# Kernel optimization log

Hardware: AMD Instinct MI355X
Metric: run time of the kernel (lower is better)

## Reference

```python
import jax, jax.numpy as jnp
import numpy as np

B, N = 16, 2048
NOTE, BEAT_H, MEAS_H, FINAL_H = 512, 128, 64, 128
NUM_BEATS, NUM_MEAS = 256, 64
OUT = 11            # output_size; QPM_INDEX = 0
QPM = 0


def _uniform(k, shape, fan):
    b = 1.0 / np.sqrt(fan)
    return jax.random.uniform(k, shape, jnp.float32, -b, b)


def _lstm_cell(x, h, c, wih, whh, bih, bhh):
    g = x @ wih.T + bih + h @ whh.T + bhh
    ii, ff, gg, oo = jnp.split(g, 4, axis=-1)
    c2 = jax.nn.sigmoid(ff) * c + jax.nn.sigmoid(ii) * jnp.tanh(gg)
    return jax.nn.sigmoid(oo) * jnp.tanh(c2), c2


def setup_inputs() -> dict:
    key = jax.random.key(0)
    ks = jax.random.split(key, 20)
    note_emb = jax.random.normal(ks[0], (B, N, NOTE), jnp.float32)
    beat_emb = jax.random.normal(ks[1], (B, NUM_BEATS, BEAT_H), jnp.float32)
    measure_emb = jax.random.normal(ks[2], (B, NUM_MEAS, MEAS_H), jnp.float32)
    beat_numbers = jnp.sort(jax.random.randint(ks[3], (B, N), 0, NUM_BEATS), axis=1)
    measure_numbers = beat_numbers // (NUM_BEATS // NUM_MEAS)
    tin = BEAT_H + MEAS_H + 1 + (OUT - 1)   # beat-tempo LSTM input size
    fin = NOTE + BEAT_H + MEAS_H + OUT      # final LSTM input size
    d = OUT - 1
    return {
        "note_emb": note_emb, "beat_emb": beat_emb, "measure_emb": measure_emb,
        "beat_numbers": beat_numbers, "measure_numbers": measure_numbers,
        "Wa": _uniform(ks[4], (d, d), d), "ba": _uniform(ks[5], (d,), d),
        "ctx": _uniform(ks[6], (d,), d),
        "Wih_t": _uniform(ks[7], (4 * BEAT_H, tin), BEAT_H),
        "Whh_t": _uniform(ks[8], (4 * BEAT_H, BEAT_H), BEAT_H),
        "bih_t": _uniform(ks[9], (4 * BEAT_H,), BEAT_H),
        "bhh_t": _uniform(ks[10], (4 * BEAT_H,), BEAT_H),
        "Wih_f": _uniform(ks[11], (4 * FINAL_H, fin), FINAL_H),
        "Whh_f": _uniform(ks[12], (4 * FINAL_H, FINAL_H), FINAL_H),
        "bih_f": _uniform(ks[13], (4 * FINAL_H,), FINAL_H),
        "bhh_f": _uniform(ks[14], (4 * FINAL_H,), FINAL_H),
        "W_fc": _uniform(ks[15], (d, FINAL_H), FINAL_H),
        "b_fc": _uniform(ks[16], (d,), FINAL_H),
        "W_tfc": _uniform(ks[17], (1, BEAT_H), BEAT_H),
        "b_tfc": _uniform(ks[18], (1,), BEAT_H),
    }


def _decode(note_emb, beat_emb, measure_emb, beat_numbers, measure_numbers,
            Wa, ba, ctx, Wih_t, Whh_t, bih_t, bhh_t,
            Wih_f, Whh_f, bih_f, bhh_f, W_fc, b_fc, W_tfc, b_tfc):
    Bn, Nn = note_emb.shape[0], note_emb.shape[1]
    d = W_fc.shape[0]  # OUT - 1
    zs_beat = jnp.maximum(beat_numbers - beat_numbers[:, :1], 0)
    zs_meas = jnp.maximum(measure_numbers - measure_numbers[:, :1], 0)
    diff = jnp.diff(beat_numbers, axis=1)
    # beat_changed: first step forced to 1, then diff of beat numbers
    changed_all = jnp.concatenate([jnp.ones((Bn, 1), diff.dtype), diff], axis=1) > 0
    pos = jnp.arange(Nn)
    bidx = jnp.arange(Bn)

    carry0 = (
        jnp.zeros((Bn, BEAT_H)), jnp.zeros((Bn, BEAT_H)),        # tempo h, c
        jnp.zeros((Bn, FINAL_H)), jnp.zeros((Bn, FINAL_H)),      # final h, c
        jnp.zeros((Bn, d + 1)),                                   # prev_out
        jnp.zeros((Bn, beat_emb.shape[1], d)),                    # beat_results
        jnp.zeros((Bn, Nn, d + 1)),                               # out_total
    )

    def step(carry, i):
        th, tc, fh, fc_, prev_out, beat_results, out_total = carry
        changed = changed_all[:, i]                                # [B] bool
        # --- get_beat_corresp_out: notes j < i in the beat just finished ---
        prev_beat = beat_numbers[:, jnp.maximum(i - 1, 0)]         # [B]
        note_mask = (beat_numbers == prev_beat[:, None]) & (pos[None, :] < i)
        x = out_total[:, :, QPM + 1:]                              # [B,N,d]
        sim = (x @ Wa.T + ba) @ ctx                                # [B,N]
        sim = jnp.where(note_mask, sim, -1e9)
        w = jax.nn.softmax(sim, axis=1)
        result_node = jnp.einsum('bn,bnd->bd', w, x)
        result_node = jnp.where(note_mask.any(axis=1)[:, None], result_node, 0.0)
        cb = zs_beat[:, i]
        cm = zs_meas[:, i]
        # scatter result_node into beat_results only for batches whose beat changed
        old = beat_results[bidx, cb]
        beat_results = beat_results.at[bidx, cb].set(
            jnp.where(changed[:, None], result_node, old))
        # --- beat tempo RNN step (only applied where changed) ---
        tempo_in = jnp.concatenate([
            beat_emb[bidx, cb], measure_emb[bidx, cm],
            prev_out[:, QPM:QPM + 1], beat_results[bidx, cb]], axis=-1)
        th2, tc2 = _lstm_cell(tempo_in, th, tc, Wih_t, Whh_t, bih_t, bhh_t)
        th = jnp.where(changed[:, None], th2, th)
        tc = jnp.where(changed[:, None], tc2, tc)
        tmp_tempo = th2 @ W_tfc.T + b_tfc                          # [B,1]
        prev_out = prev_out.at[:, QPM:QPM + 1].set(
            jnp.where(changed[:, None], tmp_tempo, prev_out[:, QPM:QPM + 1]))
        # --- final note-level LSTM step (all batches) ---
        fin_in = jnp.concatenate([
            note_emb[:, i], beat_emb[bidx, cb], measure_emb[bidx, cm], prev_out], axis=-1)
        fh, fc_ = _lstm_cell(fin_in, fh, fc_, Wih_f, Whh_f, bih_f, bhh_f)
        out = fh @ W_fc.T + b_fc                                   # [B,d]
        prev_out = jnp.concatenate([prev_out[:, :QPM + 1], out], axis=-1)
        out_total = out_total.at[:, i].set(prev_out)
        return (th, tc, fh, fc_, prev_out, beat_results, out_total), None

    carry, _ = jax.lax.scan(step, carry0, jnp.arange(Nn))
    out_total = carry[-1]
    # zero out padded notes (note embedding all-zero rows)
    pad = (note_emb.sum(-1) == 0)[:, :, None]
    return jnp.where(pad, 0.0, out_total)


def reference(note_emb, beat_emb, measure_emb, beat_numbers, measure_numbers,
              Wa, ba, ctx, Wih_t, Whh_t, bih_t, bhh_t,
              Wih_f, Whh_f, bih_f, bhh_f, W_fc, b_fc, W_tfc, b_tfc):
    return _decode(note_emb, beat_emb, measure_emb, beat_numbers, measure_numbers,
                   Wa, ba, ctx, Wih_t, Whh_t, bih_t, bhh_t,
                   Wih_f, Whh_f, bih_f, bhh_f, W_fc, b_fc, W_tfc, b_tfc)
```

## Files before the change

### kernel.cpp

```cpp
#include <hip/hip_runtime.h>
#include <cstdint>
#include <cstddef>

#define B_      16
#define N_      2048
#define NOTE_   512
#define BEAT_H_ 128
#define MEAS_H_ 64
#define NBEATS_ 256
#define NMEAS_  64
#define OUT_    11
#define D_      10

typedef float f32x4 __attribute__((ext_vector_type(4)));
typedef unsigned int u32x4 __attribute__((ext_vector_type(4)));
typedef _Float16 h2v __attribute__((ext_vector_type(2)));

__device__ __forceinline__ float fexp2_(float x) {
#if __has_builtin(__builtin_amdgcn_exp2f)
    return __builtin_amdgcn_exp2f(x);
#else
    return exp2f(x);
#endif
}
__device__ __forceinline__ float frcp_(float x) {
#if __has_builtin(__builtin_amdgcn_rcpf)
    return __builtin_amdgcn_rcpf(x);
#else
    return 1.0f / x;
#endif
}
__device__ __forceinline__ float sigm_(float x) {
    return frcp_(1.0f + fexp2_(-1.4426950408889634f * x));
}
__device__ __forceinline__ float tanh_(float x) {
    return 1.0f - 2.0f * frcp_(fexp2_(2.8853900817779268f * x) + 1.0f);
}

__device__ __forceinline__ float dot2f_(unsigned wu, unsigned hu, float c) {
    union { unsigned u; h2v h; } a, bb;
    a.u = wu; bb.u = hu;
#if __has_builtin(__builtin_amdgcn_fdot2)
    return __builtin_amdgcn_fdot2(a.h, bb.h, c, false);
#else
    return c + (float)a.h[0] * (float)bb.h[0] + (float)a.h[1] * (float)bb.h[1];
#endif
}

#define BAR_LDS() asm volatile("s_waitcnt lgkmcnt(0)\n\ts_barrier" ::: "memory")

__device__ __forceinline__ void gstore16(void* p, _Float16 v) {
    *(__attribute__((address_space(1))) _Float16*)p = v;
}

__device__ __align__(16) _Float16 g_w_i16[512 * 128];
__device__ float g_bias_eff[512];
__device__ float g_wtail0[512];
__device__ __align__(16) _Float16 g_wht_i16[512 * 128];

__global__ __launch_bounds__(256) void pad_k(const float* __restrict__ note,
                                             int* __restrict__ padf) {
    int wave = threadIdx.x >> 6, lane = threadIdx.x & 63;
    int r = blockIdx.x * 4 + wave;
    const float* row = note + ((size_t)r << 9);
    float s = 0.f;
#pragma unroll
    for (int u = 0; u < 8; ++u) s += row[lane + (u << 6)];
#pragma unroll
    for (int off = 32; off; off >>= 1) s += __shfl_xor(s, off, 64);
    if (lane == 0) padf[r] = (s == 0.0f) ? 1 : 0;
}

__global__ __launch_bounds__(128) void fold_whh(
    const float* __restrict__ Whh_f, const float* __restrict__ Wih_f,
    const float* __restrict__ W_fc, const float* __restrict__ b_fc) {
    int gr = blockIdx.x;
    int t = threadIdx.x;
    __shared__ float tail[OUT_];
    if (t < OUT_) tail[t] = Wih_f[(size_t)gr * 715 + 704 + t];
    __syncthreads();
    float m = Whh_f[(size_t)gr * 128 + t];
#pragma unroll
    for (int d = 0; d < D_; ++d) m += tail[1 + d] * W_fc[d * 128 + t];
    int g = gr >> 7, e = gr & 127;
    int half = g >> 1, slot = g & 1;
    int gl = ((e >> 5) << 6) + (e & 31) + (half << 5);
    int k = slot * 16 + (t >> 3);
    g_w_i16[(size_t)(k * 256 + gl) * 8 + (t & 7)] = (_Float16)m;
    if (t == 0) {
        float bb = 0.f;
#pragma unroll
        for (int d = 0; d < D_; ++d) bb += tail[1 + d] * b_fc[d];
        g_bias_eff[gr] = bb;
        g_wtail0[gr] = tail[0];
    }
}

__global__ __launch_bounds__(128) void fold_wht(const float* __restrict__ Whh_t) {
    int gr = blockIdx.x, t = threadIdx.x;
    int g = gr >> 7, e = gr & 127;
    int half = g >> 1, slot = g & 1;
    int gl = ((e >> 5) << 6) + (e & 31) + (half << 5);
    int k = slot * 16 + (t >> 3);
    g_wht_i16[(size_t)(k * 256 + gl) * 8 + (t & 7)] = (_Float16)Whh_t[(size_t)gr * 128 + t];
}

__global__ __launch_bounds__(256) void tempo_pre_k(
    const float* __restrict__ beat, const float* __restrict__ meas,
    const int* __restrict__ bnum, const int* __restrict__ mnum,
    const float* __restrict__ Wih_t, const float* __restrict__ bih_t,
    const float* __restrict__ bhh_t, float* __restrict__ tpre) {
    __shared__ float sin_[16][192];
    int b = blockIdx.x, qt = blockIdx.y;
    int t = threadIdx.x;
    int bn0 = bnum[b << 11], mn0 = mnum[b << 11];
    for (int idx = t; idx < 16 * 192; idx += 256) {
        int qq = idx / 192, kk = idx - qq * 192;
        int q = qt * 16 + qq;
        float v;
        if (kk < 128) {
            v = beat[(size_t)(b * NBEATS_ + q) * 128 + kk];
        } else {
            int cm = ((q + bn0) >> 2) - mn0;
            if (cm > 63) cm = 63;
            if (cm < 0) cm = 0;
            v = meas[(size_t)(b * NMEAS_ + cm) * 64 + (kk - 128)];
        }
        sin_[qq][kk] = v;
    }
    __syncthreads();
    for (int half = 0; half < 2; ++half) {
        int c = t + half * 256;
        int j = ((c & 3) << 7) | (c >> 2);
        const float* wr = Wih_t + (size_t)j * 203;
        float bias = bih_t[j] + bhh_t[j];
        float acc[16] = {};
        for (int k = 0; k < 192; ++k) {
            float w = wr[k];
#pragma unroll
            for (int qq = 0; qq < 16; ++qq) acc[qq] += w * sin_[qq][k];
        }
        for (int qq = 0; qq < 16; ++qq)
            tpre[(size_t)(b * NBEATS_ + qt * 16 + qq) * 512 + c] = acc[qq] + bias;
    }
}

__global__ __launch_bounds__(256) void fin_pre_gemm(
    const float* __restrict__ note, const float* __restrict__ beat,
    const float* __restrict__ meas, const int* __restrict__ bnum,
    const int* __restrict__ mnum, const float* __restrict__ Wih_f,
    const float* __restrict__ bih_f, const float* __restrict__ bhh_f,
    float* __restrict__ finp) {
    __shared__ float As[16][64];
    __shared__ float Bs[16][64];
    int t = threadIdx.x;
    int r0 = blockIdx.x * 64;
    int j0 = blockIdx.y * 64;

    int am = t >> 2, alane = t & 3;
    int r = r0 + am;
    int b = r >> 11;
    int rb = b << 11;
    int cb = bnum[r] - bnum[rb];
    int cm = mnum[r] - mnum[rb];
    const float* arow_note = note + ((size_t)r << 9);
    const float* arow_beat = beat + ((size_t)(b * NBEATS_ + cb) << 7);
    const float* arow_meas = meas + ((size_t)(b * NMEAS_ + cm) << 6);

    int jj = t >> 2, blane = t & 3;
    int cB = j0 + jj;
    int jB = ((cB & 3) << 7) | (cB >> 2);
    const float* brow = Wih_f + (size_t)jB * 715;

    int tm0 = (t & 15) * 4, tn0 = (t >> 4) * 4;
    float acc[4][4] = {};

    for (int k0 = 0; k0 < 704; k0 += 16) {
        int ka = k0 + alane * 4;
        float4 av;
        if (ka < 512)      av = *(const float4*)(arow_note + ka);
        else if (ka < 640) av = *(const float4*)(arow_beat + (ka - 512));
        else               av = *(const float4*)(arow_meas + (ka - 640));
        int kb = k0 + blane * 4;
        float b0 = brow[kb], b1 = brow[kb + 1], b2 = brow[kb + 2], b3 = brow[kb + 3];
        __syncthreads();
        As[alane * 4 + 0][am] = av.x;
        As[alane * 4 + 1][am] = av.y;
        As[alane * 4 + 2][am] = av.z;
        As[alane * 4 + 3][am] = av.w;
        Bs[blane * 4 + 0][jj] = b0;
        Bs[blane * 4 + 1][jj] = b1;
        Bs[blane * 4 + 2][jj] = b2;
        Bs[blane * 4 + 3][jj] = b3;
        __syncthreads();
#pragma unroll
        for (int kk = 0; kk < 16; ++kk) {
            float4 a4 = *(const float4*)&As[kk][tm0];
            float4 b4 = *(const float4*)&Bs[kk][tn0];
            float aa[4] = {a4.x, a4.y, a4.z, a4.w};
            float bb[4] = {b4.x, b4.y, b4.z, b4.w};
#pragma unroll
            for (int mi = 0; mi < 4; ++mi)
#pragma unroll
                for (int ni = 0; ni < 4; ++ni) acc[mi][ni] += aa[mi] * bb[ni];
        }
    }
    float bias[4], beff[4];
#pragma unroll
    for (int ni = 0; ni < 4; ++ni) {
        int c = j0 + tn0 + ni;
        int j = ((c & 3) << 7) | (c >> 2);
        bias[ni] = bih_f[j] + bhh_f[j];
        beff[ni] = g_bias_eff[j];
    }
#pragma unroll
    for (int mi = 0; mi < 4; ++mi) {
        int rr = r0 + tm0 + mi;
        float eb = (rr & 2047) ? 1.0f : 0.0f;
        float4 o;
        o.x = acc[mi][0] + bias[0] + eb * beff[0];
        o.y = acc[mi][1] + bias[1] + eb * beff[1];
        o.z = acc[mi][2] + bias[2] + eb * beff[2];
        o.w = acc[mi][3] + bias[3] + eb * beff[3];
        *(float4*)(finp + ((size_t)rr << 9) + j0 + tn0) = o;
    }
}

__global__ __launch_bounds__(256)
__attribute__((amdgpu_waves_per_eu(1, 1)))
void decode_seq(
    float* finp,
    const float* __restrict__ tpre, const int* __restrict__ bnum,
    const float* __restrict__ Wih_t,
    const float* __restrict__ W_fc, const float* __restrict__ b_fc,
    const float* __restrict__ W_tfc, const float* __restrict__ b_tfc,
    const float* __restrict__ Wa, const float* __restrict__ ba,
    const float* __restrict__ ctx, float* __restrict__ tval) {
    __shared__ __align__(16) u32x4 wht_i_s[32 * 256];
    __shared__ __align__(16) _Float16 hbc16[2][128];
    __shared__ __align__(16) _Float16 ht16_s[128];
    __shared__ __align__(16) _Float16 u16_s[128];
    __shared__ __align__(16) float hA_s[128];
    __shared__ __align__(16) float s_w_s[1024];
    __shared__ float wfcT[128][12];
    __shared__ float bfc_s[12];
    __shared__ float v_s[12];
    __shared__ float cur_res[12];
    __shared__ float pred_s[4];
    __shared__ float sc_s[4];
    __shared__ unsigned short run_start_s[300];
    __shared__ short run_cb_s[300];
    __shared__ int nruns_s;

    const int t = threadIdx.x, l = t & 63, wid = t >> 6;
    const int b = blockIdx.x;
    const int half = l >> 5;
    const int e = wid * 32 + (l & 31);
    const int rowA = (half * 2) * 128 + e;
    const int rowB = (half * 2 + 1) * 128 + e;
    const float kmul = half ? 2.0f : 1.0f;
    const float badd = half ? -1.0f : 0.0f;

    const float* finb = finp + ((size_t)b << 11) * 512;
    char* hg = (char*)finb;
    const int colByte = (e << 4) + (half << 3);

    {
        const u32x4* src = (const u32x4*)g_wht_i16;
#pragma unroll
        for (int k2 = 0; k2 < 32; ++k2) wht_i_s[k2 * 256 + t] = src[k2 * 256 + t];
    }

    u32x4 wreg[32];
    {
        const u32x4* gw = (const u32x4*)g_w_i16;
#pragma unroll
        for (int k = 0; k < 32; ++k) wreg[k] = gw[k * 256 + t];
    }
    asm volatile("" : "+v"(wreg[0]), "+v"(wreg[1]), "+v"(wreg[2]), "+v"(wreg[3]),
                      "+v"(wreg[4]), "+v"(wreg[5]), "+v"(wreg[6]), "+v"(wreg[7]));
    asm volatile("" : "+v"(wreg[8]), "+v"(wreg[9]), "+v"(wreg[10]), "+v"(wreg[11]),
                      "+v"(wreg[12]), "+v"(wreg[13]), "+v"(wreg[14]), "+v"(wreg[15]));
    asm volatile("" : "+v"(wreg[16]), "+v"(wreg[17]), "+v"(wreg[18]), "+v"(wreg[19]),
                      "+v"(wreg[20]), "+v"(wreg[21]), "+v"(wreg[22]), "+v"(wreg[23]));
    asm volatile("" : "+v"(wreg[24]), "+v"(wreg[25]), "+v"(wreg[26]), "+v"(wreg[27]),
                      "+v"(wreg[28]), "+v"(wreg[29]), "+v"(wreg[30]), "+v"(wreg[31]));

    const float wt0A = g_wtail0[rowA];
    const float wt0B = g_wtail0[rowB];
    const float wtfc_r = W_tfc[e];
    const float btfc_r = b_tfc[0];
    float wiht0A = Wih_t[(size_t)rowA * 203 + 192];
    float wiht0B = Wih_t[(size_t)rowB * 203 + 192];
    float wihtdA[D_], wihtdB[D_];
#pragma unroll
    for (int d = 0; d < D_; ++d) {
        wihtdA[d] = Wih_t[(size_t)rowA * 203 + 193 + d];
        wihtdB[d] = Wih_t[(size_t)rowB * 203 + 193 + d];
    }

    for (int k = t; k < 128 * D_; k += 256) {
        int d = k >> 7, r = k & 127;
        wfcT[r][d] = W_fc[k];
    }
    if (t < 128) {
        hbc16[0][t] = (_Float16)0.f;
        hbc16[1][t] = (_Float16)0.f;
        ht16_s[t] = (_Float16)0.f;
    }
    if (t < D_) {
        bfc_s[t] = b_fc[t];
        cur_res[t] = 0.f;
        float vv = 0.f;
        for (int m = 0; m < D_; ++m) vv += ctx[m] * Wa[m * D_ + t];
        v_s[t] = vv;
    }
    if (t == 10) {
        float cc = 0.f;
        for (int m = 0; m < D_; ++m) cc += ba[m] * ctx[m];
        sc_s[0] = cc;
    }
    const int* bnb = bnum + (b << 11);
    int bn0 = bnb[0];
    int base = t * 8;
    int bv[8];
#pragma unroll
    for (int j = 0; j < 8; ++j) bv[j] = bnb[base + j];
    int prevv = base ? bnb[base - 1] : (bv[0] - 1);
    int c = 0;
    {
        int vv = prevv;
#pragma unroll
        for (int j = 0; j < 8; ++j) { c += (bv[j] != vv); vv = bv[j]; }
    }
    ((int*)s_w_s)[t] = c;
    __syncthreads();
    if (t == 0) {
        float c1v = sc_s[0];
        for (int d = 0; d < D_; ++d) c1v += bfc_s[d] * v_s[d];
        sc_s[3] = c1v;
    }
    if (t < 128) {
        float uu = 0.f;
#pragma unroll
        for (int d = 0; d < D_; ++d) uu += v_s[d] * wfcT[t][d];
        u16_s[t] = (_Float16)uu;
    }
    {
        int incl = c;
#pragma unroll
        for (int off = 1; off < 64; off <<= 1) {
            int n = __shfl_up(incl, off, 64);
            if (l >= off) incl += n;
        }
        if (l == 63) ((int*)s_w_s)[512 + wid] = incl;
        __syncthreads();
        int woff = 0;
        for (int w = 0; w < wid; ++w) woff += ((int*)s_w_s)[512 + w];
        int O = woff + incl - c;
        int vv = prevv;
#pragma unroll
        for (int j = 0; j < 8; ++j) {
            if (bv[j] != vv) {
                run_start_s[O] = (unsigned short)(base + j);
                run_cb_s[O] = (short)(bv[j] - bn0);
                O++;
            }
            vv = bv[j];
        }
        if (t == 0)
            nruns_s = ((int*)s_w_s)[512] + ((int*)s_w_s)[513] +
                      ((int*)s_w_s)[514] + ((int*)s_w_s)[515];
    }
    __syncthreads();
    const int nruns_r = nruns_s;

    float2 gf_cur = *(const float2*)((const char*)finb + colByte);
    float2 tp_cur = *(const float2*)((const char*)(tpre + (size_t)(b * NBEATS_) * 512) + colByte);
    int cur_run = -1, next_start = 0, run_s = 0, S_prev = 0;
    int pb = 0;
    float cf_r = 0.f, ct_r = 0.f;
    float prev0_r = 0.f;

#pragma unroll 1
    for (int i = 0; i < N_; ++i) {
        const bool changed = (i == next_start);
        if (changed) {
            ++cur_run;
            S_prev = run_s;
            run_s = i;
            next_start = (cur_run + 1 < nruns_r) ? (int)run_start_s[cur_run + 1] : (N_ * 2);
        }
        int inx = (i + 1 < N_) ? (i + 1) : i;
        float2 gf_nxt = *(const float2*)((const char*)finb + (size_t)inx * 2048 + colByte);

        float a0 = 0.f, a1 = 0.f, a2 = 0.f, a3 = 0.f;
        float b0 = 0.f, b1 = 0.f, b2 = 0.f, b3 = 0.f;
        {
            const u32x4* hq = (const u32x4*)&hbc16[pb][0];
#pragma unroll
            for (int k = 0; k < 16; ++k) {
                u32x4 H = hq[k];
                a0 = dot2f_(wreg[k].x, H.x, a0);
                a1 = dot2f_(wreg[k].y, H.y, a1);
                a2 = dot2f_(wreg[k].z, H.z, a2);
                a3 = dot2f_(wreg[k].w, H.w, a3);
                b0 = dot2f_(wreg[16 + k].x, H.x, b0);
                b1 = dot2f_(wreg[16 + k].y, H.y, b1);
                b2 = dot2f_(wreg[16 + k].z, H.z, b2);
                b3 = dot2f_(wreg[16 + k].w, H.w, b3);
            }
        }
        const float baseA = gf_cur.x + ((a0 + a1) + (a2 + a3));
        const float baseB = gf_cur.y + ((b0 + b1) + (b2 + b3));
        gf_cur = gf_nxt;
        float gA, gB, tv;

        if (!changed) {
            gA = baseA + wt0A * prev0_r;
            gB = baseB + wt0B * prev0_r;
            tv = prev0_r;
        } else {
            float t0 = 0.f, t1 = 0.f, t2 = 0.f, t3 = 0.f;
            float u0 = 0.f, u1 = 0.f, u2 = 0.f, u3 = 0.f;
            {
                const u32x4* htq = (const u32x4*)ht16_s;
#pragma unroll
                for (int k = 0; k < 16; ++k) {
                    u32x4 HT = htq[k];
                    u32x4 WA = wht_i_s[k * 256 + t];
                    u32x4 WB = wht_i_s[(16 + k) * 256 + t];
                    t0 = dot2f_(WA.x, HT.x, t0);
                    t1 = dot2f_(WA.y, HT.y, t1);
                    t2 = dot2f_(WA.z, HT.z, t2);
                    t3 = dot2f_(WA.w, HT.w, t3);
                    u0 = dot2f_(WB.x, HT.x, u0);
                    u1 = dot2f_(WB.y, HT.y, u1);
                    u2 = dot2f_(WB.z, HT.z, u2);
                    u3 = dot2f_(WB.w, HT.w, u3);
                }
            }
            float gtA = tp_cur.x + ((t0 + t1) + (t2 + t3)) + wiht0A * prev0_r;
            float gtB = tp_cur.y + ((u0 + u1) + (u2 + u3)) + wiht0B * prev0_r;
            if (cur_run + 1 < nruns_r) {
                int cb2 = (int)run_cb_s[cur_run + 1];
                tp_cur = *(const float2*)((const char*)(tpre + (size_t)(b * NBEATS_ + cb2) * 512) + colByte);
            }

            if (wid == 0) {
                int Lc = i - S_prev;
                if (Lc > 1024) Lc = 1024;
                const char* hgB = hg + (size_t)S_prev * 2048;
                const float c1 = sc_s[3];
                float lmax = -1e30f;
                for (int j = l; j < Lc; j += 64) {
                    const u32x4* hrow = (const u32x4*)(hgB + (size_t)j * 2048);
                    const u32x4* uq = (const u32x4*)u16_s;
                    float s0 = 0.f, s1 = 0.f, s2 = 0.f, s3 = 0.f;
#pragma unroll
                    for (int k = 0; k < 16; ++k) {
                        u32x4 hv = hrow[k], uv = uq[k];
                        s0 = dot2f_(hv.x, uv.x, s0);
                        s1 = dot2f_(hv.y, uv.y, s1);
                        s2 = dot2f_(hv.z, uv.z, s2);
                        s3 = dot2f_(hv.w, uv.w, s3);
                    }
                    float s = c1 + ((s0 + s1) + (s2 + s3));
                    s_w_s[j] = s;
                    lmax = fmaxf(lmax, s);
                }
#pragma unroll
                for (int off = 32; off; off >>= 1)
                    lmax = fmaxf(lmax, __shfl_xor(lmax, off, 64));
                float lsum = 0.f;
                for (int j = l; j < Lc; j += 64) {
                    float w = fexp2_(1.4426950408889634f * (s_w_s[j] - lmax));
                    s_w_s[j] = w;
                    lsum += w;
                }
#pragma unroll
                for (int off = 32; off; off >>= 1) lsum += __shfl_xor(lsum, off, 64);
                float inv = (Lc > 0) ? (1.0f / lsum) : 0.f;
                float hA0 = 0.f, hA1 = 0.f;
                for (int j = 0; j < Lc; ++j) {
                    unsigned hv = *(const unsigned*)(hgB + (size_t)j * 2048 + (l << 2));
                    float w = s_w_s[j];
                    union { unsigned u; _Float16 h[2]; } hu; hu.u = hv;
                    hA0 += w * (float)hu.h[0];
                    hA1 += w * (float)hu.h[1];
                }
                hA_s[2 * l] = hA0 * inv;
                hA_s[2 * l + 1] = hA1 * inv;
                int dd = l >> 3, rl = l & 7, d2 = 8 + dd;
                float po1 = 0.f, po2 = 0.f;
                for (int k2 = 0; k2 < 16; ++k2) {
                    int r = rl + (k2 << 3);
                    float hv = hA_s[r];
                    po1 += hv * wfcT[r][dd];
                    if (d2 < D_) po2 += hv * wfcT[r][d2];
                }
                po1 += __shfl_xor(po1, 1, 64); po1 += __shfl_xor(po1, 2, 64); po1 += __shfl_xor(po1, 4, 64);
                po2 += __shfl_xor(po2, 1, 64); po2 += __shfl_xor(po2, 2, 64); po2 += __shfl_xor(po2, 4, 64);
                if (rl == 0) {
                    cur_res[dd] = (Lc > 0) ? (po1 + bfc_s[dd]) : 0.f;
                    if (d2 < D_) cur_res[d2] = (Lc > 0) ? (po2 + bfc_s[d2]) : 0.f;
                }
            }
            BAR_LDS();
#pragma unroll
            for (int d = 0; d < D_; ++d) {
                float cr = cur_res[d];
                gtA += wihtdA[d] * cr;
                gtB += wihtdB[d] * cr;
            }
            float actA = fmaf(kmul, sigm_(kmul * gtA), badd);
            float actB = sigm_(gtB);
            float shA = __shfl_xor(actA, 32, 64);
            float shB = __shfl_xor(actB, 32, 64);
            float p = 0.f;
            if (l < 32) {
                float c2 = actB * ct_r + actA * shA;
                float h2 = shB * tanh_(c2);
                ct_r = c2;
                ht16_s[e] = (_Float16)h2;
                p = h2 * wtfc_r;
            }
            p += __shfl_xor(p, 1, 64);
            p += __shfl_xor(p, 2, 64);
            p += __shfl_xor(p, 4, 64);
            p += __shfl_xor(p, 8, 64);
            p += __shfl_xor(p, 16, 64);
            if (l == 0) pred_s[wid] = p;
            BAR_LDS();
            float tnew = btfc_r + pred_s[0] + pred_s[1] + pred_s[2] + pred_s[3];
            prev0_r = tnew;
            tv = tnew;
            gA = baseA + wt0A * tnew;
            gB = baseB + wt0B * tnew;
        }

        {
            float actA = fmaf(kmul, sigm_(kmul * gA), badd);
            float actB = sigm_(gB);
            float shA = __shfl_xor(actA, 32, 64);
            float shB = __shfl_xor(actB, 32, 64);
            if (l < 32) {
                float c2 = actB * cf_r + actA * shA;
                float h2 = shB * tanh_(c2);
                cf_r = c2;
                hbc16[pb ^ 1][e] = (_Float16)h2;
                gstore16(hg + ((size_t)i << 11) + (e << 1), (_Float16)h2);
            }
        }
        if (t == 0) tval[(b << 11) + i] = tv;
        if (i + 1 == next_start) __syncthreads();
        else BAR_LDS();
        pb ^= 1;
    }
}

__global__ __launch_bounds__(256) void out_k(
    const float* __restrict__ finp, const float* __restrict__ tval,
    const int* __restrict__ padf, const float* __restrict__ W_fc,
    const float* __restrict__ b_fc, float* __restrict__ out) {
    int g = blockIdx.x * 256 + threadIdx.x;
    int row = g >> 4, slot = g & 15;
    if (row >= B_ * N_) return;
    int pd = padf[row];
    float* orow = out + (size_t)row * OUT_;
    if (slot == 10) {
        orow[0] = pd ? 0.f : tval[row];
        return;
    }
    if (slot > 10) return;
    const unsigned* h2 = (const unsigned*)(finp + (size_t)row * 512);
    const float* wr = W_fc + slot * 128;
    float acc = b_fc[slot];
#pragma unroll 8
    for (int k = 0; k < 64; ++k) {
        union { unsigned u; _Float16 h[2]; } hv; hv.u = h2[k];
        acc += (float)hv.h[0] * wr[2 * k] + (float)hv.h[1] * wr[2 * k + 1];
    }
    orow[1 + slot] = pd ? 0.f : acc;
}

extern "C" void kernel_launch(void* const* d_in, const int* in_sizes, int n_in,
                              void* d_out, int out_size, void* d_ws, size_t ws_size,
                              hipStream_t stream) {
    const float* note  = (const float*)d_in[0];
    const float* beat  = (const float*)d_in[1];
    const float* meas  = (const float*)d_in[2];
    const int*   bnum  = (const int*)d_in[3];
    const int*   mnum  = (const int*)d_in[4];
    const float* Wa    = (const float*)d_in[5];
    const float* ba    = (const float*)d_in[6];
    const float* ctx   = (const float*)d_in[7];
    const float* Wih_t = (const float*)d_in[8];
    const float* Whh_t = (const float*)d_in[9];
    const float* bih_t = (const float*)d_in[10];
    const float* bhh_t = (const float*)d_in[11];
    const float* Wih_f = (const float*)d_in[12];
    const float* Whh_f = (const float*)d_in[13];
    const float* bih_f = (const float*)d_in[14];
    const float* bhh_f = (const float*)d_in[15];
    const float* W_fc  = (const float*)d_in[16];
    const float* b_fc  = (const float*)d_in[17];
    const float* W_tfc = (const float*)d_in[18];
    const float* b_tfc = (const float*)d_in[19];
    float* out = (float*)d_out;

    char* ws = (char*)d_ws;
    float* finp = (float*)ws;
    float* tpre = (float*)(ws + (size_t)64 * 1024 * 1024);
    int*   padf = (int*)(ws + (size_t)72 * 1024 * 1024);
    float* tval = (float*)(ws + (size_t)73 * 1024 * 1024);

    pad_k<<<8192, 256, 0, stream>>>(note, padf);
    fold_whh<<<512, 128, 0, stream>>>(Whh_f, Wih_f, W_fc, b_fc);
    fold_wht<<<512, 128, 0, stream>>>(Whh_t);
    tempo_pre_k<<<dim3(16, 16), 256, 0, stream>>>(beat, meas, bnum, mnum, Wih_t,
                                                  bih_t, bhh_t, tpre);
    fin_pre_gemm<<<dim3(512, 8), 256, 0, stream>>>(note, beat, meas, bnum, mnum,
                                                   Wih_f, bih_f, bhh_f, finp);
    decode_seq<<<16, 256, 0, stream>>>(finp, tpre, bnum, Wih_t,
                                       W_fc, b_fc, W_tfc, b_tfc, Wa, ba, ctx,
                                       tval);
    out_k<<<2048, 256, 0, stream>>>(finp, tval, padf, W_fc, b_fc, out);
}
```

Before: 3.895 ms.

## Double-buffer precomputed gate rows into LDS with async global-to-LDS loads

Instead of issuing a global load for each note's precomputed input-gate row inside the serial recurrence, each block now prefetches 16 rows at a time into a double-buffered LDS staging area with global_load_lds, reading the current row from LDS. This is meant to take global-memory latency off the per-step critical path of the sequential LSTM. To free LDS for the staging buffers, the beat-LSTM hidden weights are now read from global memory on beat-change steps, which adds latency to those steps. The attention weighted-sum loop is also unrolled by two. The change relies on the async LDS loads having completed by the chunk-boundary barrier.

```diff
diff --git a/kernel.cpp b/kernel.cpp
--- a/kernel.cpp
+++ b/kernel.cpp
@@ -236,7 +236,7 @@
     const float* __restrict__ W_tfc, const float* __restrict__ b_tfc,
     const float* __restrict__ Wa, const float* __restrict__ ba,
     const float* __restrict__ ctx, float* __restrict__ tval) {
-    __shared__ __align__(16) u32x4 wht_i_s[32 * 256];
+    __shared__ __align__(16) float stage_s[2][16 * 512];
     __shared__ __align__(16) _Float16 hbc16[2][128];
     __shared__ __align__(16) _Float16 ht16_s[128];
     __shared__ __align__(16) _Float16 u16_s[128];
@@ -263,12 +263,20 @@
 
     const float* finb = finp + ((size_t)b << 11) * 512;
     char* hg = (char*)finb;
-    const int colByte = (e << 4) + (half << 3);
+    const int colf = (e << 2) + (half << 1);
 
     {
-        const u32x4* src = (const u32x4*)g_wht_i16;
-#pragma unroll
-        for (int k2 = 0; k2 < 32; ++k2) wht_i_s[k2 * 256 + t] = src[k2 * 256 + t];
+        const char* gsrc = (const char*)finb;
+        char* ldst = (char*)(&stage_s[0][0]);
+#pragma unroll
+        for (int n = 0; n < 8; ++n) {
+            int m = wid * 8 + n;
+            int off = m << 10;
+            __builtin_amdgcn_global_load_lds(
+                (const __attribute__((address_space(1))) unsigned*)(gsrc + off + (l << 4)),
+                (__attribute__((address_space(3))) unsigned*)(ldst + off),
+                16, 0, 0);
+        }
     }
 
     u32x4 wreg[32];
@@ -375,187 +383,219 @@
     __syncthreads();
     const int nruns_r = nruns_s;
 
-    float2 gf_cur = *(const float2*)((const char*)finb + colByte);
-    float2 tp_cur = *(const float2*)((const char*)(tpre + (size_t)(b * NBEATS_) * 512) + colByte);
+    float2 tp_cur = *(const float2*)(tpre + (size_t)(b * NBEATS_) * 512 + colf);
     int cur_run = -1, next_start = 0, run_s = 0, S_prev = 0;
-    int pb = 0;
+    int pb = 0, buf = 0;
     float cf_r = 0.f, ct_r = 0.f;
     float prev0_r = 0.f;
 
 #pragma unroll 1
-    for (int i = 0; i < N_; ++i) {
-        const bool changed = (i == next_start);
-        if (changed) {
-            ++cur_run;
-            S_prev = run_s;
-            run_s = i;
-            next_start = (cur_run + 1 < nruns_r) ? (int)run_start_s[cur_run + 1] : (N_ * 2);
-        }
-        int inx = (i + 1 < N_) ? (i + 1) : i;
-        float2 gf_nxt = *(const float2*)((const char*)finb + (size_t)inx * 2048 + colByte);
-
-        float a0 = 0.f, a1 = 0.f, a2 = 0.f, a3 = 0.f;
-        float b0 = 0.f, b1 = 0.f, b2 = 0.f, b3 = 0.f;
-        {
-            const u32x4* hq = (const u32x4*)&hbc16[pb][0];
-#pragma unroll
-            for (int k = 0; k < 16; ++k) {
-                u32x4 H = hq[k];
-                a0 = dot2f_(wreg[k].x, H.x, a0);
-                a1 = dot2f_(wreg[k].y, H.y, a1);
-                a2 = dot2f_(wreg[k].z, H.z, a2);
-                a3 = dot2f_(wreg[k].w, H.w, a3);
-                b0 = dot2f_(wreg[16 + k].x, H.x, b0);
-                b1 = dot2f_(wreg[16 + k].y, H.y, b1);
-                b2 = dot2f_(wreg[16 + k].z, H.z, b2);
-                b3 = dot2f_(wreg[16 + k].w, H.w, b3);
+    for (int ch = 0; ch < 128; ++ch) {
+        if (ch + 1 < 128) {
+            const char* gsrc = (const char*)finb + ((size_t)(ch + 1) << 15);
+            char* ldst = (char*)(&stage_s[buf ^ 1][0]);
+#pragma unroll
+            for (int n = 0; n < 8; ++n) {
+                int m = wid * 8 + n;
+                int off = m << 10;
+                __builtin_amdgcn_global_load_lds(
+                    (const __attribute__((address_space(1))) unsigned*)(gsrc + off + (l << 4)),
+                    (__attribute__((address_space(3))) unsigned*)(ldst + off),
+                    16, 0, 0);
             }
         }
-        const float baseA = gf_cur.x + ((a0 + a1) + (a2 + a3));
-        const float baseB = gf_cur.y + ((b0 + b1) + (b2 + b3));
-        gf_cur = gf_nxt;
-        float gA, gB, tv;
-
-        if (!changed) {
-            gA = baseA + wt0A * prev0_r;
-            gB = baseB + wt0B * prev0_r;
-            tv = prev0_r;
-        } else {
-            float t0 = 0.f, t1 = 0.f, t2 = 0.f, t3 = 0.f;
-            float u0 = 0.f, u1 = 0.f, u2 = 0.f, u3 = 0.f;
+#pragma unroll 1
+        for (int q = 0; q < 16; ++q) {
+            const int i = (ch << 4) | q;
+            const bool changed = (i == next_start);
+            if (changed) {
+                ++cur_run;
+                S_prev = run_s;
+                run_s = i;
+                next_start = (cur_run + 1 < nruns_r) ? (int)run_start_s[cur_run + 1] : (N_ * 2);
+            }
+            const float2 gp = *(const float2*)&stage_s[buf][(q << 9) + colf];
+
+            float a0 = 0.f, a1 = 0.f, a2 = 0.f, a3 = 0.f;
+            float b0 = 0.f, b1 = 0.f, b2 = 0.f, b3 = 0.f;
             {
-                const u32x4* htq = (const u32x4*)ht16_s;
+                const u32x4* hq = (const u32x4*)&hbc16[pb][0];
 #pragma unroll
                 for (int k = 0; k < 16; ++k) {
-                    u32x4 HT = htq[k];
-                    u32x4 WA = wht_i_s[k * 256 + t];
-                    u32x4 WB = wht_i_s[(16 + k) * 256 + t];
-                    t0 = dot2f_(WA.x, HT.x, t0);
-                    t1 = dot2f_(WA.y, HT.y, t1);
-                    t2 = dot2f_(WA.z, HT.z, t2);
-                    t3 = dot2f_(WA.w, HT.w, t3);
-                    u0 = dot2f_(WB.x, HT.x, u0);
-                    u1 = dot2f_(WB.y, HT.y, u1);
-                    u2 = dot2f_(WB.z, HT.z, u2);
-                    u3 = dot2f_(WB.w, HT.w, u3);
+                    u32x4 H = hq[k];
+                    a0 = dot2f_(wreg[k].x, H.x, a0);
+                    a1 = dot2f_(wreg[k].y, H.y, a1);
+                    a2 = dot2f_(wreg[k].z, H.z, a2);
+                    a3 = dot2f_(wreg[k].w, H.w, a3);
+                    b0 = dot2f_(wreg[16 + k].x, H.x, b0);
+                    b1 = dot2f_(wreg[16 + k].y, H.y, b1);
+                    b2 = dot2f_(wreg[16 + k].z, H.z, b2);
+                    b3 = dot2f_(wreg[16 + k].w, H.w, b3);
                 }
             }
-            float gtA = tp_cur.x + ((t0 + t1) + (t2 + t3)) + wiht0A * prev0_r;
-            float gtB = tp_cur.y + ((u0 + u1) + (u2 + u3)) + wiht0B * prev0_r;
-            if (cur_run + 1 < nruns_r) {
-                int cb2 = (int)run_cb_s[cur_run + 1];
-                tp_cur = *(const float2*)((const char*)(tpre + (size_t)(b * NBEATS_ + cb2) * 512) + colByte);
+            const float baseA = gp.x + ((a0 + a1) + (a2 + a3));
+            const float baseB = gp.y + ((b0 + b1) + (b2 + b3));
+            float gA, gB, tv;
+
+            if (!changed) {
+                gA = baseA + wt0A * prev0_r;
+                gB = baseB + wt0B * prev0_r;
+                tv = prev0_r;
+            } else {
+                float t0 = 0.f, t1 = 0.f, t2 = 0.f, t3 = 0.f;
+                float u0 = 0.f, u1 = 0.f, u2 = 0.f, u3 = 0.f;
+                {
+                    const u32x4* htq = (const u32x4*)ht16_s;
+                    const u32x4* __restrict__ gwt = (const u32x4*)g_wht_i16;
+#pragma unroll
+                    for (int k = 0; k < 16; ++k) {
+                        u32x4 HT = htq[k];
+                        u32x4 WA = gwt[k * 256 + t];
+                        u32x4 WB = gwt[(16 + k) * 256 + t];
+                        t0 = dot2f_(WA.x, HT.x, t0);
+                        t1 = dot2f_(WA.y, HT.y, t1);
+                        t2 = dot2f_(WA.z, HT.z, t2);
+                        t3 = dot2f_(WA.w, HT.w, t3);
+                        u0 = dot2f_(WB.x, HT.x, u0);
+                        u1 = dot2f_(WB.y, HT.y, u1);
+                        u2 = dot2f_(WB.z, HT.z, u2);
+                        u3 = dot2f_(WB.w, HT.w, u3);
+                    }
+                }
+                float gtA = tp_cur.x + ((t0 + t1) + (t2 + t3)) + wiht0A * prev0_r;
+                float gtB = tp_cur.y + ((u0 + u1) + (u2 + u3)) + wiht0B * prev0_r;
+                if (cur_run + 1 < nruns_r) {
+                    int cb2 = (int)run_cb_s[cur_run + 1];
+                    tp_cur = *(const float2*)(tpre + (size_t)(b * NBEATS_ + cb2) * 512 + colf);
+                }
+
+                if (wid == 0) {
+                    int Lc = i - S_prev;
+                    if (Lc > 1024) Lc = 1024;
+                    const char* hgB = hg + (size_t)S_prev * 2048;
+                    const float c1 = sc_s[3];
+                    float lmax = -1e30f;
+                    for (int j = l; j < Lc; j += 64) {
+                        const u32x4* hrow = (const u32x4*)(hgB + (size_t)j * 2048);
+                        const u32x4* uq = (const u32x4*)u16_s;
+                        float s0 = 0.f, s1 = 0.f, s2 = 0.f, s3 = 0.f;
+#pragma unroll
+                        for (int k = 0; k < 16; ++k) {
+                            u32x4 hv = hrow[k], uv = uq[k];
+                            s0 = dot2f_(hv.x, uv.x, s0);
+                            s1 = dot2f_(hv.y, uv.y, s1);
+                            s2 = dot2f_(hv.z, uv.z, s2);
+                            s3 = dot2f_(hv.w, uv.w, s3);
+                        }
+                        float s = c1 + ((s0 + s1) + (s2 + s3));
+                        s_w_s[j] = s;
+                        lmax = fmaxf(lmax, s);
+                    }
+#pragma unroll
+                    for (int off = 32; off; off >>= 1)
+                        lmax = fmaxf(lmax, __shfl_xor(lmax, off, 64));
+                    float lsum = 0.f;
+                    for (int j = l; j < Lc; j += 64) {
+                        float w = fexp2_(1.4426950408889634f * (s_w_s[j] - lmax));
+                        s_w_s[j] = w;
+                        lsum += w;
+                    }
+#pragma unroll
+                    for (int off = 32; off; off >>= 1) lsum += __shfl_xor(lsum, off, 64);
+                    float inv = (Lc > 0) ? (1.0f / lsum) : 0.f;
+                    float hA0 = 0.f, hA1 = 0.f, hB0 = 0.f, hB1 = 0.f;
+                    int jj = 0;
+                    for (; jj + 1 < Lc; jj += 2) {
+                        unsigned hv0 = *(const unsigned*)(hgB + (size_t)jj * 2048 + (l << 2));
+                        unsigned hv1 = *(const unsigned*)(hgB + (size_t)(jj + 1) * 2048 + (l << 2));
+                        float w0 = s_w_s[jj], w1 = s_w_s[jj + 1];
+                        union { unsigned u; _Float16 h[2]; } x0, x1;
+                        x0.u = hv0; x1.u = hv1;
+                        hA0 += w0 * (float)x0.h[0];
+                        hA1 += w0 * (float)x0.h[1];
+                        hB0 += w1 * (float)x1.h[0];
+                        hB1 += w1 * (float)x1.h[1];
+                    }
+                    if (jj < Lc) {
+                        unsigned hv0 = *(const unsigned*)(hgB + (size_t)jj * 2048 + (l << 2));
+                        float w0 = s_w_s[jj];
+                        union { unsigned u; _Float16 h[2]; } x0; x0.u = hv0;
+                        hA0 += w0 * (float)x0.h[0];
+                        hA1 += w0 * (float)x0.h[1];
+                    }
+                    hA_s[2 * l] = (hA0 + hB0) * inv;
+                    hA_s[2 * l + 1] = (hA1 + hB1) * inv;
+                    int dd = l >> 3, rl = l & 7, d2 = 8 + dd;
+                    float po1 = 0.f, po2 = 0.f;
+#pragma unroll
+                    for (int k2 = 0; k2 < 16; ++k2) {
+                        int r = rl + (k2 << 3);
+                        float hv = hA_s[r];
+                        po1 += hv * wfcT[r][dd];
+                        if (d2 < D_) po2 += hv * wfcT[r][d2];
+                    }
+                    po1 += __shfl_xor(po1, 1, 64); po1 += __shfl_xor(po1, 2, 64); po1 += __shfl_xor(po1, 4, 64);
+                    po2 += __shfl_xor(po2, 1, 64); po2 += __shfl_xor(po2, 2, 64); po2 += __shfl_xor(po2, 4, 64);
+                    if (rl == 0) {
+                        cur_res[dd] = (Lc > 0) ? (po1 + bfc_s[dd]) : 0.f;
+                        if (d2 < D_) cur_res[d2] = (Lc > 0) ? (po2 + bfc_s[d2]) : 0.f;
+                    }
+                }
+                BAR_LDS();
+#pragma unroll
+                for (int d = 0; d < D_; ++d) {
+                    float cr = cur_res[d];
+                    gtA += wihtdA[d] * cr;
+                    gtB += wihtdB[d] * cr;
+                }
+                float actA = fmaf(kmul, sigm_(kmul * gtA), badd);
+                float actB = sigm_(gtB);
+                float shA = __shfl_xor(actA, 32, 64);
+                float shB = __shfl_xor(actB, 32, 64);
+                float p = 0.f;
+                if (l < 32) {
+                    float c2 = actB * ct_r + actA * shA;
+                    float h2 = shB * tanh_(c2);
+                    ct_r = c2;
+                    ht16_s[e] = (_Float16)h2;
+                    p = h2 * wtfc_r;
+                }
+                p += __shfl_xor(p, 1, 64);
+                p += __shfl_xor(p, 2, 64);
+                p += __shfl_xor(p, 4, 64);
+                p += __shfl_xor(p, 8, 64);
+                p += __shfl_xor(p, 16, 64);
+                if (l == 0) pred_s[wid] = p;
+                BAR_LDS();
+                float tnew = btfc_r + pred_s[0] + pred_s[1] + pred_s[2] + pred_s[3];
+                prev0_r = tnew;
+                tv = tnew;
+                gA = baseA + wt0A * tnew;
+                gB = baseB + wt0B * tnew;
             }
 
-            if (wid == 0) {
-                int Lc = i - S_prev;
-                if (Lc > 1024) Lc = 1024;
-                const char* hgB = hg + (size_t)S_prev * 2048;
-                const float c1 = sc_s[3];
-                float lmax = -1e30f;
-                for (int j = l; j < Lc; j += 64) {
-                    const u32x4* hrow = (const u32x4*)(hgB + (size_t)j * 2048);
-                    const u32x4* uq = (const u32x4*)u16_s;
-                    float s0 = 0.f, s1 = 0.f, s2 = 0.f, s3 = 0.f;
-#pragma unroll
-                    for (int k = 0; k < 16; ++k) {
-                        u32x4 hv = hrow[k], uv = uq[k];
-                        s0 = dot2f_(hv.x, uv.x, s0);
-                        s1 = dot2f_(hv.y, uv.y, s1);
-                        s2 = dot2f_(hv.z, uv.z, s2);
-                        s3 = dot2f_(hv.w, uv.w, s3);
-                    }
-                    float s = c1 + ((s0 + s1) + (s2 + s3));
-                    s_w_s[j] = s;
-                    lmax = fmaxf(lmax, s);
-                }
-#pragma unroll
-                for (int off = 32; off; off >>= 1)
-                    lmax = fmaxf(lmax, __shfl_xor(lmax, off, 64));
-                float lsum = 0.f;
-                for (int j = l; j < Lc; j += 64) {
-                    float w = fexp2_(1.4426950408889634f * (s_w_s[j] - lmax));
-                    s_w_s[j] = w;
-                    lsum += w;
-                }
-#pragma unroll
-                for (int off = 32; off; off >>= 1) lsum += __shfl_xor(lsum, off, 64);
-                float inv = (Lc > 0) ? (1.0f / lsum) : 0.f;
-                float hA0 = 0.f, hA1 = 0.f;
-                for (int j = 0; j < Lc; ++j) {
-                    unsigned hv = *(const unsigned*)(hgB + (size_t)j * 2048 + (l << 2));
-                    float w = s_w_s[j];
-                    union { unsigned u; _Float16 h[2]; } hu; hu.u = hv;
-                    hA0 += w * (float)hu.h[0];
-                    hA1 += w * (float)hu.h[1];
-                }
-                hA_s[2 * l] = hA0 * inv;
-                hA_s[2 * l + 1] = hA1 * inv;
-                int dd = l >> 3, rl = l & 7, d2 = 8 + dd;
-                float po1 = 0.f, po2 = 0.f;
-                for (int k2 = 0; k2 < 16; ++k2) {
-                    int r = rl + (k2 << 3);
-                    float hv = hA_s[r];
-                    po1 += hv * wfcT[r][dd];
-                    if (d2 < D_) po2 += hv * wfcT[r][d2];
-                }
-                po1 += __shfl_xor(po1, 1, 64); po1 += __shfl_xor(po1, 2, 64); po1 += __shfl_xor(po1, 4, 64);
-                po2 += __shfl_xor(po2, 1, 64); po2 += __shfl_xor(po2, 2, 64); po2 += __shfl_xor(po2, 4, 64);
-                if (rl == 0) {
-                    cur_res[dd] = (Lc > 0) ? (po1 + bfc_s[dd]) : 0.f;
-                    if (d2 < D_) cur_res[d2] = (Lc > 0) ? (po2 + bfc_s[d2]) : 0.f;
+            {
+                float actA = fmaf(kmul, sigm_(kmul * gA), badd);
+                float actB = sigm_(gB);
+                float shA = __shfl_xor(actA, 32, 64);
+                float shB = __shfl_xor(actB, 32, 64);
+                if (l < 32) {
+                    float c2 = actB * cf_r + actA * shA;
+                    float h2 = shB * tanh_(c2);
+                    cf_r = c2;
+                    hbc16[pb ^ 1][e] = (_Float16)h2;
+                    gstore16(hg + ((size_t)i << 11) + (e << 1), (_Float16)h2);
                 }
             }
-            BAR_LDS();
-#pragma unroll
-            for (int d = 0; d < D_; ++d) {
-                float cr = cur_res[d];
-                gtA += wihtdA[d] * cr;
-                gtB += wihtdB[d] * cr;
+            if (t == 0) tval[(b << 11) + i] = tv;
+            {
+                bool nextch = (i + 1 == next_start);
+                if (nextch || q == 15) __syncthreads();
+                else BAR_LDS();
             }
-            float actA = fmaf(kmul, sigm_(kmul * gtA), badd);
-            float actB = sigm_(gtB);
-            float shA = __shfl_xor(actA, 32, 64);
-            float shB = __shfl_xor(actB, 32, 64);
-            float p = 0.f;
-            if (l < 32) {
-                float c2 = actB * ct_r + actA * shA;
-                float h2 = shB * tanh_(c2);
-                ct_r = c2;
-                ht16_s[e] = (_Float16)h2;
-                p = h2 * wtfc_r;
-            }
-            p += __shfl_xor(p, 1, 64);
-            p += __shfl_xor(p, 2, 64);
-            p += __shfl_xor(p, 4, 64);
-            p += __shfl_xor(p, 8, 64);
-            p += __shfl_xor(p, 16, 64);
-            if (l == 0) pred_s[wid] = p;
-            BAR_LDS();
-            float tnew = btfc_r + pred_s[0] + pred_s[1] + pred_s[2] + pred_s[3];
-            prev0_r = tnew;
-            tv = tnew;
-            gA = baseA + wt0A * tnew;
-            gB = baseB + wt0B * tnew;
-        }
-
-        {
-            float actA = fmaf(kmul, sigm_(kmul * gA), badd);
-            float actB = sigm_(gB);
-            float shA = __shfl_xor(actA, 32, 64);
-            float shB = __shfl_xor(actB, 32, 64);
-            if (l < 32) {
-                float c2 = actB * cf_r + actA * shA;
-                float h2 = shB * tanh_(c2);
-                cf_r = c2;
-                hbc16[pb ^ 1][e] = (_Float16)h2;
-                gstore16(hg + ((size_t)i << 11) + (e << 1), (_Float16)h2);
-            }
-        }
-        if (t == 0) tval[(b << 11) + i] = tv;
-        if (i + 1 == next_start) __syncthreads();
-        else BAR_LDS();
-        pb ^= 1;
+            pb ^= 1;
+        }
+        buf ^= 1;
     }
 }
 
```

Result: slower. 4.456 ms (+14.4%).
